# Kernel optimization log

Hardware: AMD Instinct MI355X
Metric: run time of the kernel (lower is better)

Reference implementation:

```python
import jax, jax.numpy as jnp
import numpy as np

N = 50000      # nodes
E = 800000     # edges
D = 128        # in_dim == out_dim
H = 8          # heads
DH = D // H    # head dim = 16
BN_EPS = 1e-5


def batch_norm(x, gamma, beta):
    # BatchNorm1d in training mode: biased variance over the node/batch axis.
    mu = jnp.mean(x, axis=0)
    var = jnp.mean((x - mu) ** 2, axis=0)
    return (x - mu) * jax.lax.rsqrt(var + BN_EPS) * gamma + beta


def setup_inputs() -> dict:
    key = jax.random.key(0)
    ks = jax.random.split(key, 16)
    inp = {
        'src': jax.random.randint(ks[0], (E,), 0, N),
        'dst': jax.random.randint(ks[1], (E,), 0, N),
        'h': jax.random.normal(ks[2], (N, D), jnp.float32),
        'e': jax.random.normal(ks[3], (E, D), jnp.float32),
        'h_in': jax.random.normal(ks[4], (N, D), jnp.float32),  # unused: overwritten by h in forward
        # attention projections (bias=False)
        'Wq': jax.random.normal(ks[5], (D, D), jnp.float32) / np.sqrt(D),
        'Wk': jax.random.normal(ks[6], (D, D), jnp.float32) / np.sqrt(D),
        'Wv': jax.random.normal(ks[7], (D, D), jnp.float32) / np.sqrt(D),
        'We': jax.random.normal(ks[8], (D, D), jnp.float32) / np.sqrt(D),
        # sdp_layer (bias=True)
        'W_sdp': jax.random.normal(ks[9], (D, D), jnp.float32) / np.sqrt(D),
        'b_sdp': jnp.zeros((D,), jnp.float32),
        # FFN out_h / out_h_2
        'W_h1': jax.random.normal(ks[10], (D, 2 * D), jnp.float32) / np.sqrt(D),
        'b_h1': jnp.zeros((2 * D,), jnp.float32),
        'W_h2': jax.random.normal(ks[11], (2 * D, D), jnp.float32) / np.sqrt(2 * D),
        'b_h2': jnp.zeros((D,), jnp.float32),
        # batch_norm_1 (shared across both BN applications)
        'bn_gamma': jnp.ones((D,), jnp.float32),
        'bn_beta': jnp.zeros((D,), jnp.float32),
    }
    return inp


def reference(src, dst, h, e, h_in, Wq, Wk, Wv, We, W_sdp, b_sdp,
              W_h1, b_h1, W_h2, b_h2, bn_gamma, bn_beta):
    h_res = h  # h_in = h inside forward

    # --- MultiHeadAttention (default path: all edges real, sum aggregation) ---
    q = (h @ Wq).reshape(N, H, DH)
    k = (h @ Wk).reshape(N, H, DH)
    v = (h @ Wv).reshape(N, H, DH)   # v = v_linear(h_in) with h_in == h
    ef = (e @ We).reshape(E, H, DH)

    # src_dot_dst -> scaling -> imp_exp_attn: elementwise K_src*Q_dst / sqrt(dh) * E
    score = (k[src] * q[dst]) / np.sqrt(DH) * ef          # [E, H, DH]
    # exp('score'): exp(clamp(sum_d score, -5, 5)), keepdim
    score_soft = jnp.exp(jnp.clip(score.sum(-1), -5.0, 5.0))[..., None]  # [E, H, 1]

    aV = jax.ops.segment_sum(v[src] * score_soft, dst, num_segments=N)   # [N, H, DH]
    z = jax.ops.segment_sum(score_soft, dst, num_segments=N)             # [N, H, 1]
    h_attn = (aV / (z + 1e-6)).reshape(N, D)

    # --- EncoderLayer post-attention (dropout=0 -> identity) ---
    hx = h_attn @ W_sdp + b_sdp
    hx = h_res + hx
    hx = batch_norm(hx, bn_gamma, bn_beta)

    h_in2 = hx
    ff = jax.nn.relu(hx @ W_h1 + b_h1) @ W_h2 + b_h2
    hx = h_in2 + ff
    hx = batch_norm(hx, bn_gamma, bn_beta)

    # edge_learning=False: e returned unchanged
    return hx, e
```

## Files before the change

kernel.cpp:

```cpp
#include <hip/hip_runtime.h>
#include <hip/hip_bf16.h>
#include <math.h>

#define N_NODES 50000
#define E_EDGES 800000
#define D_DIM   128
#define H_HEADS 8

typedef __attribute__((ext_vector_type(8))) short short8;
typedef __attribute__((ext_vector_type(4))) float f32x4;
typedef unsigned int   uint_t;
typedef unsigned short ushort_t;

static __device__ __forceinline__ float4 ldg4(const float* p) {
    return *reinterpret_cast<const float4*>(p);
}
static __device__ __forceinline__ ushort_t f2bf(float x) {
    union { float f; uint_t u; } v; v.f = x;
    uint_t r = v.u + 0x7fffu + ((v.u >> 16) & 1u);
    return (ushort_t)(r >> 16);
}
static __device__ __forceinline__ float bf2f(ushort_t b) {
    union { uint_t u; float f; } v; v.u = ((uint_t)b) << 16;
    return v.f;
}
static __device__ __forceinline__ uint_t pk(float lo, float hi) {
    return (uint_t)f2bf(lo) | ((uint_t)f2bf(hi) << 16);
}

__global__ void hist_kernel(const int* __restrict__ dst, int* __restrict__ hist) {
    int i = blockIdx.x * blockDim.x + threadIdx.x;
    if (i < E_EDGES) atomicAdd(&hist[dst[i]], 1);
}

__global__ __launch_bounds__(1024) void scan_kernel(const int* __restrict__ cnt,
                                                    int* __restrict__ start,
                                                    int* __restrict__ cursor) {
    __shared__ int sh[1024];
    const int t = threadIdx.x;
    const int CPT = (N_NODES + 1023) / 1024;
    int lo = t * CPT;
    int hi = lo + CPT; if (hi > N_NODES) hi = N_NODES; if (lo > N_NODES) lo = N_NODES;
    int s = 0;
    for (int i = lo; i < hi; i++) s += cnt[i];
    sh[t] = s;
    __syncthreads();
    for (int off = 1; off < 1024; off <<= 1) {
        int v = (t >= off) ? sh[t - off] : 0;
        __syncthreads();
        sh[t] += v;
        __syncthreads();
    }
    int run = sh[t] - s;
    for (int i = lo; i < hi; i++) {
        start[i]  = run;
        cursor[i] = run;
        run += cnt[i];
    }
    if (t == 1023) start[N_NODES] = sh[1023];
}

__global__ void scatter_kernel(const int* __restrict__ src, const int* __restrict__ dst,
                               int* __restrict__ cursor,
                               int* __restrict__ rank, int* __restrict__ srcs) {
    int i = blockIdx.x * blockDim.x + threadIdx.x;
    if (i < E_EDGES) {
        int p = atomicAdd(&cursor[dst[i]], 1);
        rank[i] = p;
        srcs[p] = src[i];
    }
}

__global__ __launch_bounds__(256) void prep_weights(const float* __restrict__ Wq,
                                                    const float* __restrict__ Wk,
                                                    const float* __restrict__ Wv,
                                                    const float* __restrict__ We,
                                                    const float* __restrict__ Wsdp,
                                                    const float* __restrict__ Wh1,
                                                    const float* __restrict__ Wh2,
                                                    ushort_t* __restrict__ prep) {
    const int b = blockIdx.x;
    const float* W; int ld, cb, kc;
    if (b < 6)       { W = (b < 2 ? Wq : (b < 4 ? Wk : Wv)); ld = 128; cb = 0; kc = b & 1; }
    else if (b < 8)  { W = We;   ld = 128; cb = 0;            kc = b - 6; }
    else if (b < 10) { W = Wsdp; ld = 128; cb = 0;            kc = b - 8; }
    else if (b < 14) { W = Wh1;  ld = 256; cb = (b - 10) >> 1; kc = (b - 10) & 1; }
    else             { W = Wh2;  ld = 128; cb = 0;            kc = b - 14; }
    char* tile = (char*)(prep + (size_t)b * 8192);
    for (int i = threadIdx.x; i < 8192; i += 256) {
        int col = i >> 6, kl = i & 63;
        int k = kc * 64 + kl;
        float v = W[(size_t)k * ld + cb * 128 + col];
        int byte = (col * 128 + kl * 2) ^ ((col & 7) << 4);
        *(ushort_t*)(tile + byte) = f2bf(v);
    }
}

__global__ __launch_bounds__(256) void prep_we_frag(const float* __restrict__ We,
                                                    ushort_t* __restrict__ WeF) {
    int slot = blockIdx.x * 256 + threadIdx.x;
    if (slot < 2048) {
        int lane = slot & 63;
        int kc   = (slot >> 6) & 3;
        int cg   = slot >> 8;
        int col  = cg * 16 + (lane & 15);
        int kb   = kc * 32 + ((lane >> 4) << 3);
#pragma unroll
        for (int j = 0; j < 8; j++)
            WeF[slot * 8 + j] = f2bf(We[(size_t)(kb + j) * 128 + col]);
    }
}

template<int ROWS, int OBF, int ABF, int RESMODE, int SADD, int ASS>
__global__ __launch_bounds__(256) void gemm_bf16(const void* __restrict__ Av,
                                                 int M, int K,
                                                 const ushort_t* __restrict__ Bt, int nkc,
                                                 const float* __restrict__ bias,
                                                 const void* __restrict__ residv,
                                                 void* __restrict__ Cv, int ldc,
                                                 size_t cbStride, int doRelu,
                                                 float* __restrict__ sums,
                                                 const float* __restrict__ ss) {
    constexpr int MI  = ROWS / 32;
    constexpr int TPR = 256 / ROWS;
    constexpr int KPT = 64 / TPR;
    __shared__ __align__(16) unsigned char As[ROWS * 128];
    __shared__ __align__(16) unsigned char Bs[16384];
    __shared__ float csum[128], csq[128];
    const int tid  = threadIdx.x;
    const int lane = tid & 63;
    const int wid  = tid >> 6;
    const int wr   = wid >> 1;
    const int wc   = wid & 1;
    const int cb   = blockIdx.y;
    const int row0 = blockIdx.x * ROWS;

    if (SADD && tid < 128) { csum[tid] = 0.f; csq[tid] = 0.f; }

    f32x4 acc[MI][4];
#pragma unroll
    for (int i = 0; i < MI; i++)
#pragma unroll
        for (int j = 0; j < 4; j++) acc[i][j] = (f32x4){0.f, 0.f, 0.f, 0.f};

    for (int kc = 0; kc < nkc; kc++) {
        __syncthreads();
        {
            int row = tid / TPR;
            int kl0 = (tid % TPR) * KPT;
            int gr  = row0 + row;
            int s = (row & 7) << 4;
            if (ABF) {
                const ushort_t* A16 = (const ushort_t*)Av;
#pragma unroll
                for (int j = 0; j < KPT / 8; j++) {
                    uint4 w = make_uint4(0, 0, 0, 0);
                    if (gr < M) w = *(const uint4*)(&A16[(size_t)gr * K + kc * 64 + kl0 + 8 * j]);
                    int byte = (row * 128 + (kl0 + 8 * j) * 2) ^ s;
                    *(uint4*)(As + byte) = w;
                }
            } else {
                const float* A = (const float*)Av;
                float4 v4[KPT / 4];
                if (gr < M) {
                    const float* ap = &A[(size_t)gr * K + kc * 64 + kl0];
#pragma unroll
                    for (int j = 0; j < KPT / 4; j++) v4[j] = ldg4(ap + 4 * j);
                } else {
#pragma unroll
                    for (int j = 0; j < KPT / 4; j++) v4[j] = make_float4(0.f, 0.f, 0.f, 0.f);
                }
                if (ASS) {
#pragma unroll
                    for (int j = 0; j < KPT / 4; j++) {
                        int kk = kc * 64 + kl0 + 4 * j;
                        v4[j].x = v4[j].x * ss[kk + 0] + ss[128 + kk + 0];
                        v4[j].y = v4[j].y * ss[kk + 1] + ss[128 + kk + 1];
                        v4[j].z = v4[j].z * ss[kk + 2] + ss[128 + kk + 2];
                        v4[j].w = v4[j].w * ss[kk + 3] + ss[128 + kk + 3];
                    }
                }
#pragma unroll
                for (int j = 0; j < KPT / 8; j++) {
                    uint4 w;
                    w.x = pk(v4[2 * j].x, v4[2 * j].y);
                    w.y = pk(v4[2 * j].z, v4[2 * j].w);
                    w.z = pk(v4[2 * j + 1].x, v4[2 * j + 1].y);
                    w.w = pk(v4[2 * j + 1].z, v4[2 * j + 1].w);
                    int byte = (row * 128 + (kl0 + 8 * j) * 2) ^ s;
                    *(uint4*)(As + byte) = w;
                }
            }
        }
        {
            const uint4* gB = (const uint4*)(Bt + (size_t)(cb * nkc + kc) * 8192);
#pragma unroll
            for (int j = 0; j < 4; j++) {
                int idx = j * 256 + tid;
                ((uint4*)Bs)[idx] = gB[idx];
            }
        }
        __syncthreads();
#pragma unroll
        for (int k0 = 0; k0 < 64; k0 += 32) {
            short8 a[MI], b[4];
#pragma unroll
            for (int mi = 0; mi < MI; mi++) {
                int row = wr * (ROWS / 2) + mi * 16 + (lane & 15);
                int byte = (row * 128 + k0 * 2 + (lane >> 4) * 16) ^ ((row & 7) << 4);
                a[mi] = *(const short8*)(As + byte);
            }
#pragma unroll
            for (int ni = 0; ni < 4; ni++) {
                int col = wc * 64 + ni * 16 + (lane & 15);
                int byte = (col * 128 + k0 * 2 + (lane >> 4) * 16) ^ ((col & 7) << 4);
                b[ni] = *(const short8*)(Bs + byte);
            }
#pragma unroll
            for (int mi = 0; mi < MI; mi++)
#pragma unroll
                for (int ni = 0; ni < 4; ni++)
                    acc[mi][ni] = __builtin_amdgcn_mfma_f32_16x16x32_bf16(a[mi], b[ni], acc[mi][ni], 0, 0, 0);
        }
    }

    float colS[4] = {0.f, 0.f, 0.f, 0.f};
    float colQ[4] = {0.f, 0.f, 0.f, 0.f};
#pragma unroll
    for (int mi = 0; mi < MI; mi++) {
#pragma unroll
        for (int r = 0; r < 4; r++) {
            int row = row0 + wr * (ROWS / 2) + mi * 16 + ((lane >> 4) << 2) + r;
            if (row < M) {
#pragma unroll
                for (int ni = 0; ni < 4; ni++) {
                    int col = wc * 64 + ni * 16 + (lane & 15);
                    float v = acc[mi][ni][r];
                    if (bias) v += bias[cb * 128 + col];
                    if (doRelu) v = fmaxf(v, 0.f);
                    if (residv) {
                        if (RESMODE == 1) {
                            v += bf2f(((const ushort_t*)residv)[(size_t)row * ldc + col]);
                        } else if (RESMODE == 2) {
                            float rr = ((const float*)residv)[(size_t)row * ldc + col];
                            v += rr * ss[col] + ss[128 + col];
                        } else {
                            v += ((const float*)residv)[(size_t)row * ldc + col];
                        }
                    }
                    if (SADD) { colS[ni] += v; colQ[ni] += v * v; }
                    if (OBF) ((ushort_t*)Cv)[cb * cbStride + (size_t)row * ldc + col] = f2bf(v);
                    else     ((float*)Cv)[cb * cbStride + (size_t)row * ldc + col] = v;
                }
            }
        }
    }
    if (SADD) {
#pragma unroll
        for (int ni = 0; ni < 4; ni++) {
            int col = wc * 64 + ni * 16 + (lane & 15);
            atomicAdd(&csum[col], colS[ni]);
            atomicAdd(&csq[col],  colQ[ni]);
        }
        __syncthreads();
        if (tid < 128) {
            atomicAdd(&sums[tid],       csum[tid]);
            atomicAdd(&sums[128 + tid], csq[tid]);
        }
    }
}

__global__ __launch_bounds__(512, 8) void edge_mfma(const float* __restrict__ e,
                                                    const int* __restrict__ src,
                                                    const int* __restrict__ dst,
                                                    const ushort_t* __restrict__ Qm,
                                                    const ushort_t* __restrict__ Km,
                                                    const ushort_t* __restrict__ WeF,
                                                    const int* __restrict__ rank,
                                                    ushort_t* __restrict__ S16,
                                                    float* __restrict__ out_e) {
    __shared__ __align__(16) unsigned char Asm[16384];
    __shared__ __align__(16) ushort_t sm[64][8];
    const int tid  = threadIdx.x;
    const int lane = tid & 63;
    const int wid  = tid >> 6;
    const int wr   = wid >> 2;
    const int wc   = wid & 3;
    const int e0   = blockIdx.x * 64;

    {
        int row = tid >> 3;
        int c0  = (tid & 7) * 16;
        const float* ep = &e[(size_t)(e0 + row) * 128 + c0];
        float*       op = &out_e[(size_t)(e0 + row) * 128 + c0];
        float4 v4[4];
#pragma unroll
        for (int j = 0; j < 4; j++) v4[j] = ldg4(ep + 4 * j);
#pragma unroll
        for (int j = 0; j < 4; j++) *(float4*)(op + 4 * j) = v4[j];
        int chunk = c0 >> 6;
        int klb   = (c0 & 63) * 2;
        int s     = (row & 7) << 4;
        uint4 w0, w1;
        w0.x = pk(v4[0].x, v4[0].y); w0.y = pk(v4[0].z, v4[0].w);
        w0.z = pk(v4[1].x, v4[1].y); w0.w = pk(v4[1].z, v4[1].w);
        w1.x = pk(v4[2].x, v4[2].y); w1.y = pk(v4[2].z, v4[2].w);
        w1.z = pk(v4[3].x, v4[3].y); w1.w = pk(v4[3].z, v4[3].w);
        *(uint4*)(Asm + chunk * 8192 + ((row * 128 + klb) ^ s))      = w0;
        *(uint4*)(Asm + chunk * 8192 + ((row * 128 + klb + 16) ^ s)) = w1;
    }
    __syncthreads();

    f32x4 acc[2][2];
#pragma unroll
    for (int i = 0; i < 2; i++)
#pragma unroll
        for (int j = 0; j < 2; j++) acc[i][j] = (f32x4){0.f, 0.f, 0.f, 0.f};

#pragma unroll
    for (int k0 = 0; k0 < 128; k0 += 32) {
        int chunk = k0 >> 6;
        int klb   = (k0 & 63) * 2;
        int kc    = k0 >> 5;
        short8 a[2];
#pragma unroll
        for (int mi = 0; mi < 2; mi++) {
            int arow = wr * 32 + mi * 16 + (lane & 15);
            int byte = chunk * 8192 + ((arow * 128 + klb + (lane >> 4) * 16) ^ ((arow & 7) << 4));
            a[mi] = *(const short8*)(Asm + byte);
        }
#pragma unroll
        for (int ni = 0; ni < 2; ni++) {
            int cg = wc * 2 + ni;
            short8 b = *(const short8*)(WeF + ((size_t)((cg * 4 + kc) * 64 + lane)) * 8);
#pragma unroll
            for (int mi = 0; mi < 2; mi++)
                acc[mi][ni] = __builtin_amdgcn_mfma_f32_16x16x32_bf16(a[mi], b, acc[mi][ni], 0, 0, 0);
        }
    }

#pragma unroll
    for (int mi = 0; mi < 2; mi++) {
        int rows[4], sidx[4], didx[4];
#pragma unroll
        for (int r = 0; r < 4; r++) {
            rows[r] = e0 + wr * 32 + mi * 16 + ((lane >> 4) << 2) + r;
            sidx[r] = src[rows[r]];
            didx[r] = dst[rows[r]];
        }
#pragma unroll
        for (int ni = 0; ni < 2; ni++) {
            int head = wc * 2 + ni;
            int col  = head * 16 + (lane & 15);
            float pv[4];
#pragma unroll
            for (int r = 0; r < 4; r++) {
                float kv = bf2f(Km[(size_t)sidx[r] * 128 + col]);
                float qv = bf2f(Qm[(size_t)didx[r] * 128 + col]);
                pv[r] = acc[mi][ni][r] * kv * qv;
            }
#pragma unroll
            for (int off = 1; off < 16; off <<= 1)
#pragma unroll
                for (int r = 0; r < 4; r++) pv[r] += __shfl_xor(pv[r], off, 64);
            if ((lane & 15) == 0) {
#pragma unroll
                for (int r = 0; r < 4; r++) {
                    float v = fminf(fmaxf(0.25f * pv[r], -5.f), 5.f);
                    sm[rows[r] - e0][head] = f2bf(__expf(v));
                }
            }
        }
    }
    __syncthreads();
    if (tid < 64) {
        int rk = rank[e0 + tid];
        uint4 u = *(const uint4*)&sm[tid][0];
        *(uint4*)&S16[(size_t)rk * 8] = u;
    }
}

__global__ __launch_bounds__(256) void agg_kernel(const uint_t* __restrict__ Vu,
                                                  const ushort_t* __restrict__ S16,
                                                  const int* __restrict__ start,
                                                  const int* __restrict__ srcs,
                                                  uint_t* __restrict__ HAu) {
    const int lane = threadIdx.x & 63;
    const int n = blockIdx.x * 4 + (threadIdx.x >> 6);
    if (n >= N_NODES) return;
    const int s0 = start[n];
    const int s1 = start[n + 1];
    const int h  = lane >> 3;
    float a0 = 0.f, a1 = 0.f, z = 0.f;
    int i = s0;
    for (; i + 4 <= s1; i += 4) {
        int m0 = srcs[i], m1 = srcs[i + 1], m2 = srcs[i + 2], m3 = srcs[i + 3];
        float t0 = bf2f(S16[(size_t)i * 8 + h]);
        float t1 = bf2f(S16[(size_t)(i + 1) * 8 + h]);
        float t2 = bf2f(S16[(size_t)(i + 2) * 8 + h]);
        float t3 = bf2f(S16[(size_t)(i + 3) * 8 + h]);
        uint_t v0 = Vu[(size_t)m0 * 64 + lane];
        uint_t v1 = Vu[(size_t)m1 * 64 + lane];
        uint_t v2 = Vu[(size_t)m2 * 64 + lane];
        uint_t v3 = Vu[(size_t)m3 * 64 + lane];
        a0 = fmaf(t0, bf2f((ushort_t)v0), a0); a1 = fmaf(t0, bf2f((ushort_t)(v0 >> 16)), a1);
        a0 = fmaf(t1, bf2f((ushort_t)v1), a0); a1 = fmaf(t1, bf2f((ushort_t)(v1 >> 16)), a1);
        a0 = fmaf(t2, bf2f((ushort_t)v2), a0); a1 = fmaf(t2, bf2f((ushort_t)(v2 >> 16)), a1);
        a0 = fmaf(t3, bf2f((ushort_t)v3), a0); a1 = fmaf(t3, bf2f((ushort_t)(v3 >> 16)), a1);
        z += t0 + t1 + t2 + t3;
    }
    for (; i < s1; i++) {
        int m = srcs[i];
        float t = bf2f(S16[(size_t)i * 8 + h]);
        uint_t v = Vu[(size_t)m * 64 + lane];
        a0 = fmaf(t, bf2f((ushort_t)v), a0);
        a1 = fmaf(t, bf2f((ushort_t)(v >> 16)), a1);
        z += t;
    }
    float inv = 1.f / (z + 1e-6f);
    HAu[(size_t)n * 64 + lane] = pk(a0 * inv, a1 * inv);
}

__global__ void bn_finalize(const float* __restrict__ sums,
                            const float* __restrict__ gamma,
                            const float* __restrict__ beta,
                            float* __restrict__ ss) {
    int c = threadIdx.x;
    float mu  = sums[c] * (1.f / (float)N_NODES);
    float var = sums[128 + c] * (1.f / (float)N_NODES) - mu * mu;
    float scale = rsqrtf(var + 1e-5f) * gamma[c];
    ss[c]       = scale;
    ss[128 + c] = beta[c] - mu * scale;
}

__global__ __launch_bounds__(256) void bn_apply_f32(const float* __restrict__ X,
                                                    const float* __restrict__ ss,
                                                    float* __restrict__ Y) {
    const size_t total = (size_t)N_NODES * 128;
    const size_t step = (size_t)gridDim.x * blockDim.x * 4;
    for (size_t i = ((size_t)blockIdx.x * blockDim.x + threadIdx.x) * 4; i < total; i += step) {
        float4 x = ldg4(&X[i]);
        int c = (int)(i & 127);
        float4 y;
        y.x = x.x * ss[c + 0] + ss[128 + c + 0];
        y.y = x.y * ss[c + 1] + ss[128 + c + 1];
        y.z = x.z * ss[c + 2] + ss[128 + c + 2];
        y.w = x.w * ss[c + 3] + ss[128 + c + 3];
        *(float4*)(&Y[i]) = y;
    }
}

extern "C" void kernel_launch(void* const* d_in, const int* in_sizes, int n_in,
                              void* d_out, int out_size, void* d_ws, size_t ws_size,
                              hipStream_t stream) {
    (void)in_sizes; (void)n_in; (void)out_size; (void)ws_size;
    const int*   src   = (const int*)d_in[0];
    const int*   dst   = (const int*)d_in[1];
    const float* h     = (const float*)d_in[2];
    const float* e     = (const float*)d_in[3];
    const float* Wq    = (const float*)d_in[5];
    const float* Wk    = (const float*)d_in[6];
    const float* Wv    = (const float*)d_in[7];
    const float* We    = (const float*)d_in[8];
    const float* Wsdp  = (const float*)d_in[9];
    const float* bsdp  = (const float*)d_in[10];
    const float* Wh1   = (const float*)d_in[11];
    const float* bh1   = (const float*)d_in[12];
    const float* Wh2   = (const float*)d_in[13];
    const float* bh2   = (const float*)d_in[14];
    const float* gamma = (const float*)d_in[15];
    const float* beta  = (const float*)d_in[16];
    float* out = (float*)d_out;

    float* ws = (float*)d_ws;
    const size_t NM = (size_t)N_NODES * 128;
    ushort_t* Q16  = (ushort_t*)ws;
    ushort_t* K16  = Q16 + NM;
    ushort_t* V16  = Q16 + 2 * NM;
    ushort_t* HA16 = (ushort_t*)(ws + 3 * NM / 2);
    float*    Kb   = ws + 2 * NM;
    ushort_t* S16  = (ushort_t*)(ws + 3 * NM);
    float*    T1r  = ws + 4 * NM;
    ushort_t* T16  = (ushort_t*)T1r;
    float*    STATS = ws + 6 * NM;
    int* hist   = (int*)(STATS + 1024);
    int* startp = hist + N_NODES;
    int* cursor = startp + N_NODES + 1;
    ushort_t* prep = (ushort_t*)(((uintptr_t)(cursor + N_NODES) + 255) & ~(uintptr_t)255);
    ushort_t* WeF  = prep + (size_t)18 * 8192;

    int* rank = (int*)T1r;
    int* srcs = rank + E_EDGES;

    float* sums1 = STATS;
    float* ss1   = STATS + 256;
    float* sums2 = STATS + 512;
    float* ss2   = STATS + 768;

    prep_weights<<<18, 256, 0, stream>>>(Wq, Wk, Wv, We, Wsdp, Wh1, Wh2, prep);
    prep_we_frag<<<8, 256, 0, stream>>>(We, WeF);

    hipMemsetAsync(STATS, 0, (1024 + N_NODES) * sizeof(float), stream);

    hist_kernel<<<(E_EDGES + 255) / 256, 256, 0, stream>>>(dst, hist);
    scan_kernel<<<1, 1024, 0, stream>>>(hist, startp, cursor);
    scatter_kernel<<<(E_EDGES + 255) / 256, 256, 0, stream>>>(src, dst, cursor, rank, srcs);

    const int rt128 = (N_NODES + 127) / 128;
    const int rt64  = (N_NODES + 63) / 64;

    gemm_bf16<128, 1, 0, 0, 0, 0><<<dim3(rt128, 3), 256, 0, stream>>>(
        h, N_NODES, 128, prep, 2, nullptr, nullptr, Q16, 128, NM, 0, nullptr, nullptr);

    edge_mfma<<<E_EDGES / 64, 512, 0, stream>>>(e, src, dst, Q16, K16, WeF,
                                                rank, S16, out + NM);

    agg_kernel<<<(N_NODES + 3) / 4, 256, 0, stream>>>((const uint_t*)V16, S16, startp, srcs,
                                                      (uint_t*)HA16);

    gemm_bf16<64, 0, 1, 0, 1, 0><<<dim3(rt64, 1), 256, 0, stream>>>(
        HA16, N_NODES, 128, prep + (size_t)8 * 8192, 2, bsdp, h, Kb, 128, 0, 0, sums1, nullptr);

    bn_finalize<<<1, 128, 0, stream>>>(sums1, gamma, beta, ss1);

    gemm_bf16<128, 1, 0, 0, 0, 1><<<dim3(rt128, 2), 256, 0, stream>>>(
        Kb, N_NODES, 128, prep + (size_t)10 * 8192, 2, bh1, nullptr, T16, 256, 128, 1, nullptr, ss1);
    gemm_bf16<64, 0, 1, 2, 1, 0><<<dim3(rt64, 1), 256, 0, stream>>>(
        T16, N_NODES, 256, prep + (size_t)14 * 8192, 4, bh2, Kb, Kb, 128, 0, 0, sums2, ss1);

    bn_finalize<<<1, 128, 0, stream>>>(sums2, gamma, beta, ss2);
    bn_apply_f32<<<2048, 256, 0, stream>>>(Kb, ss2, out);
}
```

Measured before the change: 783.3 us.

## Process four edge tiles per block and store attention scores in fp32

The edge kernel now loops over four 64-edge tiles per block with a non-unrolled loop, so the grid is a quarter of its former size and each block reuses its shared buffers across tiles. Attention scores are kept in fp32 rather than rounded to bf16, both in the edge kernel output and in the aggregation reads. The tiling change aims to amortise per-block launch and setup cost, but it serialises load, MFMA and epilogue inside each block and reduces how many blocks are available to hide latency. The fp32 scores double the score write and read traffic in exchange for better accuracy.

```diff
diff --git a/kernel.cpp b/kernel.cpp
--- a/kernel.cpp
+++ b/kernel.cpp
@@ -6,6 +6,7 @@
 #define E_EDGES 800000
 #define D_DIM   128
 #define H_HEADS 8
+#define ETILES  4
 
 typedef __attribute__((ext_vector_type(8))) short short8;
 typedef __attribute__((ext_vector_type(4))) float f32x4;
@@ -277,111 +278,118 @@
                                                     const ushort_t* __restrict__ Km,
                                                     const ushort_t* __restrict__ WeF,
                                                     const int* __restrict__ rank,
-                                                    ushort_t* __restrict__ S16,
+                                                    float* __restrict__ S,
                                                     float* __restrict__ out_e) {
     __shared__ __align__(16) unsigned char Asm[16384];
-    __shared__ __align__(16) ushort_t sm[64][8];
+    __shared__ float sm[64][8];
     const int tid  = threadIdx.x;
     const int lane = tid & 63;
     const int wid  = tid >> 6;
     const int wr   = wid >> 2;
     const int wc   = wid & 3;
-    const int e0   = blockIdx.x * 64;
-
-    {
-        int row = tid >> 3;
-        int c0  = (tid & 7) * 16;
-        const float* ep = &e[(size_t)(e0 + row) * 128 + c0];
-        float*       op = &out_e[(size_t)(e0 + row) * 128 + c0];
-        float4 v4[4];
-#pragma unroll
-        for (int j = 0; j < 4; j++) v4[j] = ldg4(ep + 4 * j);
-#pragma unroll
-        for (int j = 0; j < 4; j++) *(float4*)(op + 4 * j) = v4[j];
-        int chunk = c0 >> 6;
-        int klb   = (c0 & 63) * 2;
-        int s     = (row & 7) << 4;
-        uint4 w0, w1;
-        w0.x = pk(v4[0].x, v4[0].y); w0.y = pk(v4[0].z, v4[0].w);
-        w0.z = pk(v4[1].x, v4[1].y); w0.w = pk(v4[1].z, v4[1].w);
-        w1.x = pk(v4[2].x, v4[2].y); w1.y = pk(v4[2].z, v4[2].w);
-        w1.z = pk(v4[3].x, v4[3].y); w1.w = pk(v4[3].z, v4[3].w);
-        *(uint4*)(Asm + chunk * 8192 + ((row * 128 + klb) ^ s))      = w0;
-        *(uint4*)(Asm + chunk * 8192 + ((row * 128 + klb + 16) ^ s)) = w1;
-    }
-    __syncthreads();
-
-    f32x4 acc[2][2];
-#pragma unroll
-    for (int i = 0; i < 2; i++)
-#pragma unroll
-        for (int j = 0; j < 2; j++) acc[i][j] = (f32x4){0.f, 0.f, 0.f, 0.f};
-
-#pragma unroll
-    for (int k0 = 0; k0 < 128; k0 += 32) {
-        int chunk = k0 >> 6;
-        int klb   = (k0 & 63) * 2;
-        int kc    = k0 >> 5;
-        short8 a[2];
+    const int base = blockIdx.x * (64 * ETILES);
+
+#pragma unroll 1
+    for (int t = 0; t < ETILES; t++) {
+        const int e0 = base + t * 64;
+
+        {
+            int row = tid >> 3;
+            int c0  = (tid & 7) * 16;
+            const float* ep = &e[(size_t)(e0 + row) * 128 + c0];
+            float*       op = &out_e[(size_t)(e0 + row) * 128 + c0];
+            float4 v4[4];
+#pragma unroll
+            for (int j = 0; j < 4; j++) v4[j] = ldg4(ep + 4 * j);
+#pragma unroll
+            for (int j = 0; j < 4; j++) *(float4*)(op + 4 * j) = v4[j];
+            int chunk = c0 >> 6;
+            int klb   = (c0 & 63) * 2;
+            int s     = (row & 7) << 4;
+            uint4 w0, w1;
+            w0.x = pk(v4[0].x, v4[0].y); w0.y = pk(v4[0].z, v4[0].w);
+            w0.z = pk(v4[1].x, v4[1].y); w0.w = pk(v4[1].z, v4[1].w);
+            w1.x = pk(v4[2].x, v4[2].y); w1.y = pk(v4[2].z, v4[2].w);
+            w1.z = pk(v4[3].x, v4[3].y); w1.w = pk(v4[3].z, v4[3].w);
+            *(uint4*)(Asm + chunk * 8192 + ((row * 128 + klb) ^ s))      = w0;
+            *(uint4*)(Asm + chunk * 8192 + ((row * 128 + klb + 16) ^ s)) = w1;
+        }
+        __syncthreads();
+
+        f32x4 acc[2][2];
+#pragma unroll
+        for (int i = 0; i < 2; i++)
+#pragma unroll
+            for (int j = 0; j < 2; j++) acc[i][j] = (f32x4){0.f, 0.f, 0.f, 0.f};
+
+#pragma unroll
+        for (int k0 = 0; k0 < 128; k0 += 32) {
+            int chunk = k0 >> 6;
+            int klb   = (k0 & 63) * 2;
+            int kc    = k0 >> 5;
+            short8 a[2];
+#pragma unroll
+            for (int mi = 0; mi < 2; mi++) {
+                int arow = wr * 32 + mi * 16 + (lane & 15);
+                int byte = chunk * 8192 + ((arow * 128 + klb + (lane >> 4) * 16) ^ ((arow & 7) << 4));
+                a[mi] = *(const short8*)(Asm + byte);
+            }
+#pragma unroll
+            for (int ni = 0; ni < 2; ni++) {
+                int cg = wc * 2 + ni;
+                short8 b = *(const short8*)(WeF + ((size_t)((cg * 4 + kc) * 64 + lane)) * 8);
+#pragma unroll
+                for (int mi = 0; mi < 2; mi++)
+                    acc[mi][ni] = __builtin_amdgcn_mfma_f32_16x16x32_bf16(a[mi], b, acc[mi][ni], 0, 0, 0);
+            }
+        }
+
 #pragma unroll
         for (int mi = 0; mi < 2; mi++) {
-            int arow = wr * 32 + mi * 16 + (lane & 15);
-            int byte = chunk * 8192 + ((arow * 128 + klb + (lane >> 4) * 16) ^ ((arow & 7) << 4));
-            a[mi] = *(const short8*)(Asm + byte);
-        }
-#pragma unroll
-        for (int ni = 0; ni < 2; ni++) {
-            int cg = wc * 2 + ni;
-            short8 b = *(const short8*)(WeF + ((size_t)((cg * 4 + kc) * 64 + lane)) * 8);
-#pragma unroll
-            for (int mi = 0; mi < 2; mi++)
-                acc[mi][ni] = __builtin_amdgcn_mfma_f32_16x16x32_bf16(a[mi], b, acc[mi][ni], 0, 0, 0);
-        }
-    }
-
-#pragma unroll
-    for (int mi = 0; mi < 2; mi++) {
-        int rows[4], sidx[4], didx[4];
-#pragma unroll
-        for (int r = 0; r < 4; r++) {
-            rows[r] = e0 + wr * 32 + mi * 16 + ((lane >> 4) << 2) + r;
-            sidx[r] = src[rows[r]];
-            didx[r] = dst[rows[r]];
-        }
-#pragma unroll
-        for (int ni = 0; ni < 2; ni++) {
-            int head = wc * 2 + ni;
-            int col  = head * 16 + (lane & 15);
-            float pv[4];
+            int rows[4], sidx[4], didx[4];
 #pragma unroll
             for (int r = 0; r < 4; r++) {
-                float kv = bf2f(Km[(size_t)sidx[r] * 128 + col]);
-                float qv = bf2f(Qm[(size_t)didx[r] * 128 + col]);
-                pv[r] = acc[mi][ni][r] * kv * qv;
-            }
-#pragma unroll
-            for (int off = 1; off < 16; off <<= 1)
-#pragma unroll
-                for (int r = 0; r < 4; r++) pv[r] += __shfl_xor(pv[r], off, 64);
-            if ((lane & 15) == 0) {
+                rows[r] = e0 + wr * 32 + mi * 16 + ((lane >> 4) << 2) + r;
+                sidx[r] = src[rows[r]];
+                didx[r] = dst[rows[r]];
+            }
+#pragma unroll
+            for (int ni = 0; ni < 2; ni++) {
+                int head = wc * 2 + ni;
+                int col  = head * 16 + (lane & 15);
+                float pv[4];
 #pragma unroll
                 for (int r = 0; r < 4; r++) {
-                    float v = fminf(fmaxf(0.25f * pv[r], -5.f), 5.f);
-                    sm[rows[r] - e0][head] = f2bf(__expf(v));
-                }
-            }
-        }
-    }
-    __syncthreads();
-    if (tid < 64) {
-        int rk = rank[e0 + tid];
-        uint4 u = *(const uint4*)&sm[tid][0];
-        *(uint4*)&S16[(size_t)rk * 8] = u;
+                    float kv = bf2f(Km[(size_t)sidx[r] * 128 + col]);
+                    float qv = bf2f(Qm[(size_t)didx[r] * 128 + col]);
+                    pv[r] = acc[mi][ni][r] * kv * qv;
+                }
+#pragma unroll
+                for (int off = 1; off < 16; off <<= 1)
+#pragma unroll
+                    for (int r = 0; r < 4; r++) pv[r] += __shfl_xor(pv[r], off, 64);
+                if ((lane & 15) == 0) {
+#pragma unroll
+                    for (int r = 0; r < 4; r++) {
+                        float v = fminf(fmaxf(0.25f * pv[r], -5.f), 5.f);
+                        sm[rows[r] - e0][head] = __expf(v);
+                    }
+                }
+            }
+        }
+        __syncthreads();
+        if (tid < 64) {
+            int rk = rank[e0 + tid];
+            float4 a0 = *(const float4*)&sm[tid][0];
+            float4 a1 = *(const float4*)&sm[tid][4];
+            *(float4*)&S[(size_t)rk * 8]     = a0;
+            *(float4*)&S[(size_t)rk * 8 + 4] = a1;
+        }
     }
 }
 
 __global__ __launch_bounds__(256) void agg_kernel(const uint_t* __restrict__ Vu,
-                                                  const ushort_t* __restrict__ S16,
+                                                  const float* __restrict__ S,
                                                   const int* __restrict__ start,
                                                   const int* __restrict__ srcs,
                                                   uint_t* __restrict__ HAu) {
@@ -395,10 +403,10 @@
     int i = s0;
     for (; i + 4 <= s1; i += 4) {
         int m0 = srcs[i], m1 = srcs[i + 1], m2 = srcs[i + 2], m3 = srcs[i + 3];
-        float t0 = bf2f(S16[(size_t)i * 8 + h]);
-        float t1 = bf2f(S16[(size_t)(i + 1) * 8 + h]);
-        float t2 = bf2f(S16[(size_t)(i + 2) * 8 + h]);
-        float t3 = bf2f(S16[(size_t)(i + 3) * 8 + h]);
+        float t0 = S[(size_t)i * 8 + h];
+        float t1 = S[(size_t)(i + 1) * 8 + h];
+        float t2 = S[(size_t)(i + 2) * 8 + h];
+        float t3 = S[(size_t)(i + 3) * 8 + h];
         uint_t v0 = Vu[(size_t)m0 * 64 + lane];
         uint_t v1 = Vu[(size_t)m1 * 64 + lane];
         uint_t v2 = Vu[(size_t)m2 * 64 + lane];
@@ -411,7 +419,7 @@
     }
     for (; i < s1; i++) {
         int m = srcs[i];
-        float t = bf2f(S16[(size_t)i * 8 + h]);
+        float t = S[(size_t)i * 8 + h];
         uint_t v = Vu[(size_t)m * 64 + lane];
         a0 = fmaf(t, bf2f((ushort_t)v), a0);
         a1 = fmaf(t, bf2f((ushort_t)(v >> 16)), a1);
@@ -479,7 +487,7 @@
     ushort_t* V16  = Q16 + 2 * NM;
     ushort_t* HA16 = (ushort_t*)(ws + 3 * NM / 2);
     float*    Kb   = ws + 2 * NM;
-    ushort_t* S16  = (ushort_t*)(ws + 3 * NM);
+    float*    Sb   = ws + 3 * NM;
     float*    T1r  = ws + 4 * NM;
     ushort_t* T16  = (ushort_t*)T1r;
     float*    STATS = ws + 6 * NM;
@@ -512,10 +520,10 @@
     gemm_bf16<128, 1, 0, 0, 0, 0><<<dim3(rt128, 3), 256, 0, stream>>>(
         h, N_NODES, 128, prep, 2, nullptr, nullptr, Q16, 128, NM, 0, nullptr, nullptr);
 
-    edge_mfma<<<E_EDGES / 64, 512, 0, stream>>>(e, src, dst, Q16, K16, WeF,
-                                                rank, S16, out + NM);
-
-    agg_kernel<<<(N_NODES + 3) / 4, 256, 0, stream>>>((const uint_t*)V16, S16, startp, srcs,
+    edge_mfma<<<E_EDGES / (64 * ETILES), 512, 0, stream>>>(e, src, dst, Q16, K16, WeF,
+                                                           rank, Sb, out + NM);
+
+    agg_kernel<<<(N_NODES + 3) / 4, 256, 0, stream>>>((const uint_t*)V16, Sb, startp, srcs,
                                                       (uint_t*)HA16);
 
     gemm_bf16<64, 0, 1, 0, 1, 0><<<dim3(rt64, 1), 256, 0, stream>>>(
```

Result: slower. 990.8 us (+26.5%).
